# Kernel tuning notes

Measured on AMD Instinct MI355X. Metric: run time of the kernel, lower is better.

Reference implementation:

```python
import jax, jax.numpy as jnp
import numpy as np

BS, NQ, DIM, HEADS, POINTS, LEVELS = 2, 4096, 768, 6, 4, 1
HD = DIM // HEADS
H = W = 64
NV = H * W
EPS = 1e-6


def setup_inputs() -> dict:
    key = jax.random.key(0)
    ks = jax.random.split(key, 16)
    s = 0.02  # param init scale
    return {
        "query": jax.random.normal(ks[0], (BS, NQ, DIM), jnp.float32),
        "reference_points": jax.random.uniform(ks[1], (BS, NQ, LEVELS, 2), jnp.float32),
        "feat": jax.random.normal(ks[2], (BS, NV, DIM), jnp.float32),
        "spatial_shapes": np.array([[H, W]], dtype=np.int64),
        "level_start_index": np.array([0], dtype=np.int64),
        "ln_w": jnp.ones((DIM,), jnp.float32),
        "ln_b": jnp.zeros((DIM,), jnp.float32),
        "vp_w": jax.random.normal(ks[3], (DIM, DIM), jnp.float32) * s,
        "vp_b": jnp.zeros((DIM,), jnp.float32),
        "off_w": jax.random.normal(ks[4], (DIM, HEADS * LEVELS * POINTS * 2), jnp.float32) * s,
        "off_b": jax.random.normal(ks[5], (HEADS * LEVELS * POINTS * 2,), jnp.float32),
        "aw_w": jax.random.normal(ks[6], (DIM, HEADS * LEVELS * POINTS), jnp.float32) * s,
        "aw_b": jnp.zeros((HEADS * LEVELS * POINTS,), jnp.float32),
        "out_w": jax.random.normal(ks[7], (DIM, DIM), jnp.float32) * s,
        "out_b": jnp.zeros((DIM,), jnp.float32),
        "gamma": jax.random.normal(ks[8], (DIM,), jnp.float32) * 0.1,
    }


def _layernorm(x, w, b):
    mu = jnp.mean(x, axis=-1, keepdims=True)
    var = jnp.mean(jnp.square(x - mu), axis=-1, keepdims=True)
    return (x - mu) * jax.lax.rsqrt(var + EPS) * w + b


def _bilinear_sample(img, loc):
    # img: (bs, heads, H, W, hd); loc: (bs, nq, heads, points, 2) in [0,1]
    # matches torch.grid_sample(align_corners=False, padding_mode='zeros')
    bs, heads, h, w, hd = img.shape
    x = loc[..., 0] * w - 0.5
    y = loc[..., 1] * h - 0.5
    x0 = jnp.floor(x)
    y0 = jnp.floor(y)
    wx = x - x0
    wy = y - y0
    x0i = x0.astype(jnp.int32)
    y0i = y0.astype(jnp.int32)
    bi = jnp.arange(bs)[:, None, None, None]
    hi = jnp.arange(heads)[None, None, :, None]

    def gather(yi, xi):
        valid = (xi >= 0) & (xi < w) & (yi >= 0) & (yi < h)
        v = img[bi, hi, jnp.clip(yi, 0, h - 1), jnp.clip(xi, 0, w - 1)]
        return v * valid[..., None].astype(img.dtype)

    v00 = gather(y0i, x0i)
    v01 = gather(y0i, x0i + 1)
    v10 = gather(y0i + 1, x0i)
    v11 = gather(y0i + 1, x0i + 1)
    wx = wx[..., None]
    wy = wy[..., None]
    return (v00 * (1 - wy) * (1 - wx) + v01 * (1 - wy) * wx
            + v10 * wy * (1 - wx) + v11 * wy * wx)


def _msda(q, value, reference_points, spatial_shapes, off_w, off_b, aw_w, aw_b, out_w, out_b):
    bs, nq, _ = q.shape
    nv = value.shape[1]
    value = value.reshape(bs, nv, HEADS, HD)
    offsets = (q @ off_w + off_b).reshape(bs, nq, HEADS, LEVELS, POINTS, 2)
    aw = jax.nn.softmax(q @ aw_w + aw_b, axis=-1).reshape(bs, nq, HEADS, LEVELS, POINTS)
    # offset_normalizer = [W_l, H_l] per level
    norm = jnp.asarray(np.asarray(spatial_shapes)[:, ::-1], jnp.float32)  # (L, 2)
    loc = reference_points[:, :, None, :, None, :] + offsets / norm[None, None, None, :, None, :]
    # loc: (bs, nq, heads, levels, points, 2)
    out = jnp.zeros((bs, nq, HEADS, HD), jnp.float32)
    start = 0
    for l in range(LEVELS):
        h_l, w_l = int(spatial_shapes[l][0]), int(spatial_shapes[l][1])
        img = value[:, start:start + h_l * w_l].reshape(bs, h_l, w_l, HEADS, HD).transpose(0, 3, 1, 2, 4)
        sampled = _bilinear_sample(img, loc[:, :, :, l])  # (bs, nq, heads, points, hd)
        out = out + jnp.einsum('bnhpd,bnhp->bnhd', sampled, aw[:, :, :, l])
        start += h_l * w_l
    return out.reshape(bs, nq, DIM) @ out_w + out_b


def reference(query, reference_points, feat, spatial_shapes, level_start_index,
              ln_w, ln_b, vp_w, vp_b, off_w, off_b, aw_w, aw_b, out_w, out_b, gamma):
    q = _layernorm(query, ln_w, ln_b)
    value = feat @ vp_w + vp_b
    attn = _msda(q, value, reference_points, spatial_shapes,
                 off_w, off_b, aw_w, aw_b, out_w, out_b)
    # identity = zeros, dropout = 0 -> attn as-is; residual scale by gamma
    return query + gamma * attn
```

## Files before the change

### kernel.cpp

```cpp
#include <hip/hip_runtime.h>
#include <hip/hip_bf16.h>
#include <math.h>

#define BSZ 2
#define NQ 4096
#define DIM 768
#define HEADS 6
#define POINTS 4
#define HD 128
#define HW_DIM 64
#define NV (HW_DIM*HW_DIM)
#define M_TOTAL (BSZ*NQ)
#define KDIM 768
#define KSPLIT 2
#define KPART (KDIM/KSPLIT)

#define BM 64
#define BN 128
#define BKK 64
#define NBLK_M (M_TOTAL/BM)
#define NBLK_N (DIM/BN)
#define GEMM_GRID (NBLK_M*NBLK_N)
#define LN_BLOCKS (M_TOTAL/4)
#define TR_BLOCKS (576+576+72)

typedef __attribute__((ext_vector_type(8))) short bf16x8;
typedef __attribute__((ext_vector_type(4))) float f32x4;
typedef unsigned int u32;
typedef unsigned short u16;

__device__ inline u16 f2bf(float f) {
    union { float f; u32 u; } v; v.f = f;
    u32 r = v.u + 0x7fffu + ((v.u >> 16) & 1u);
    return (u16)(r >> 16);
}

#define GLD16(g, l) __builtin_amdgcn_global_load_lds( \
    (const __attribute__((address_space(1))) u32*)(g), \
    (__attribute__((address_space(3))) u32*)(l), 16, 0, 0)

__global__ __launch_bounds__(256) void prep_kernel(
        const float* __restrict__ x, const float* __restrict__ lnw,
        const float* __restrict__ lnb, u16* __restrict__ q,
        const float* __restrict__ feat, u16* __restrict__ feat_bf,
        const float* __restrict__ vp_w,  u16* __restrict__ vp_wt,
        const float* __restrict__ out_w, u16* __restrict__ out_wt,
        const float* __restrict__ off_w, const float* __restrict__ aw_w,
        u16* __restrict__ oaw_wt) {
    int b = blockIdx.x;
    if (b < LN_BLOCKS) {
        int wave = threadIdx.x >> 6, lane = threadIdx.x & 63;
        int row = b * 4 + wave;
        int c = lane * 4;
        const float* xr = x + (size_t)row * DIM;
        const float* fr = feat + (size_t)row * DIM;
        float4 v0 = *(const float4*)(xr + c);
        float4 v1 = *(const float4*)(xr + c + 256);
        float4 v2 = *(const float4*)(xr + c + 512);
        float4 f0 = *(const float4*)(fr + c);
        float4 f1 = *(const float4*)(fr + c + 256);
        float4 f2 = *(const float4*)(fr + c + 512);
        u16* fb = feat_bf + (size_t)row * DIM;
        ushort4 fo;
        fo.x = f2bf(f0.x); fo.y = f2bf(f0.y); fo.z = f2bf(f0.z); fo.w = f2bf(f0.w);
        *(ushort4*)(fb + c) = fo;
        fo.x = f2bf(f1.x); fo.y = f2bf(f1.y); fo.z = f2bf(f1.z); fo.w = f2bf(f1.w);
        *(ushort4*)(fb + c + 256) = fo;
        fo.x = f2bf(f2.x); fo.y = f2bf(f2.y); fo.z = f2bf(f2.z); fo.w = f2bf(f2.w);
        *(ushort4*)(fb + c + 512) = fo;

        float s  = v0.x+v0.y+v0.z+v0.w + v1.x+v1.y+v1.z+v1.w + v2.x+v2.y+v2.z+v2.w;
        float ss = v0.x*v0.x+v0.y*v0.y+v0.z*v0.z+v0.w*v0.w
                 + v1.x*v1.x+v1.y*v1.y+v1.z*v1.z+v1.w*v1.w
                 + v2.x*v2.x+v2.y*v2.y+v2.z*v2.z+v2.w*v2.w;
        #pragma unroll
        for (int st = 1; st < 64; st <<= 1) {
            s  += __shfl_xor(s,  st, 64);
            ss += __shfl_xor(ss, st, 64);
        }
        float mean = s * (1.0f / DIM);
        float var  = ss * (1.0f / DIM) - mean * mean;
        float rstd = rsqrtf(var + 1e-6f);
        u16* qr = q + (size_t)row * DIM;
        #pragma unroll
        for (int g = 0; g < 3; g++) {
            float4 v = (g == 0) ? v0 : (g == 1) ? v1 : v2;
            int cc = c + g * 256;
            const float4 ww = *(const float4*)(lnw + cc);
            const float4 bb = *(const float4*)(lnb + cc);
            ushort4 o;
            o.x = f2bf((v.x - mean) * rstd * ww.x + bb.x);
            o.y = f2bf((v.y - mean) * rstd * ww.y + bb.y);
            o.z = f2bf((v.z - mean) * rstd * ww.z + bb.z);
            o.w = f2bf((v.w - mean) * rstd * ww.w + bb.w);
            *(ushort4*)(qr + cc) = o;
        }
    } else {
        int t = b - LN_BLOCKS;
        int z, xk, yk;
        if (t < 576)      { z = 0; xk = t % 24; yk = t / 24; }
        else if (t < 1152){ z = 1; t -= 576; xk = t % 24; yk = t / 24; }
        else              { z = 2; t -= 1152; xk = t % 3; yk = t / 3; }
        __shared__ float tile[32][33];
        int n0 = xk * 32, k0 = yk * 32;
        int tx = threadIdx.x & 31, ty = threadIdx.x >> 5;
        const float* src = (z == 0) ? vp_w : (z == 1) ? out_w : nullptr;
        u16* dst = (z == 0) ? vp_wt : (z == 1) ? out_wt : oaw_wt;
        #pragma unroll
        for (int r = 0; r < 4; r++) {
            int k = k0 + ty + r * 8, n = n0 + tx;
            float v = 0.0f;
            if (z < 2) {
                v = src[(size_t)k * DIM + n];
            } else {
                if (n < 48) v = off_w[(size_t)k * 48 + n];
                else if (n < 72) v = aw_w[(size_t)k * 24 + (n - 48)];
            }
            tile[ty + r * 8][tx] = v;
        }
        __syncthreads();
        #pragma unroll
        for (int r = 0; r < 4; r++) {
            int nn = ty + r * 8, kk = tx;
            int drow = n0 + nn;
            if (z == 2 && drow >= 80) continue;
            dst[(size_t)drow * KDIM + k0 + kk] = f2bf(tile[kk][nn]);
        }
    }
}

__device__ __forceinline__ void gemm_big_body(int b,
        const u16* __restrict__ A, const u16* __restrict__ Bt,
        const float* __restrict__ bias, void* __restrict__ Cout,
        int storeBF16, const float* __restrict__ resid,
        const float* __restrict__ gamma) {
    __shared__ u16 As[BM * BKK];
    __shared__ u16 Bs[BN * BKK];
    int tid = threadIdx.x, w = tid >> 6, lane = tid & 63;
    int lm = lane & 15, quad = lane >> 4;
    int xcd = b & 7, idx = b >> 3;
    int mb = xcd * 16 + idx / NBLK_N;
    int nb = idx % NBLK_N;
    int m0 = mb * BM, n0 = nb * BN;
    int wr = w & 1, wc = w >> 1;

    int srow = lane >> 3;
    int scol = (lane & 7) ^ srow;
    const u16* Ab = A + (size_t)m0 * KDIM;
    const u16* Bb = Bt + (size_t)n0 * KDIM;

    f32x4 acc[2][4];
    #pragma unroll
    for (int i = 0; i < 2; i++)
        #pragma unroll
        for (int j = 0; j < 4; j++) acc[i][j] = (f32x4){0.f, 0.f, 0.f, 0.f};

    const u16* aaddr[2][2];
    const u16* baddr[4][2];
    #pragma unroll
    for (int i = 0; i < 2; i++) {
        int row = wr * 32 + i * 16 + lm;
        #pragma unroll
        for (int kk = 0; kk < 2; kk++)
            aaddr[i][kk] = &As[row * BKK + (((quad + 4 * kk) ^ (row & 7)) << 3)];
    }
    #pragma unroll
    for (int j = 0; j < 4; j++) {
        int row = wc * 64 + j * 16 + lm;
        #pragma unroll
        for (int kk = 0; kk < 2; kk++)
            baddr[j][kk] = &Bs[row * BKK + (((quad + 4 * kk) ^ (row & 7)) << 3)];
    }

    for (int k0 = 0; k0 < KDIM; k0 += BKK) {
        #pragma unroll
        for (int r = 0; r < 2; r++) {
            int row = r * 32 + w * 8 + srow;
            GLD16(Ab + (size_t)row * KDIM + k0 + scol * 8, &As[(r * 32 + w * 8) * BKK]);
        }
        #pragma unroll
        for (int r = 0; r < 4; r++) {
            int row = r * 32 + w * 8 + srow;
            GLD16(Bb + (size_t)row * KDIM + k0 + scol * 8, &Bs[(r * 32 + w * 8) * BKK]);
        }
        __syncthreads();
        #pragma unroll
        for (int kk = 0; kk < 2; kk++) {
            bf16x8 af[2], bf[4];
            #pragma unroll
            for (int i = 0; i < 2; i++) af[i] = *(const bf16x8*)aaddr[i][kk];
            #pragma unroll
            for (int j = 0; j < 4; j++) bf[j] = *(const bf16x8*)baddr[j][kk];
            #pragma unroll
            for (int i = 0; i < 2; i++)
                #pragma unroll
                for (int j = 0; j < 4; j++)
                    acc[i][j] = __builtin_amdgcn_mfma_f32_16x16x32_bf16(af[i], bf[j], acc[i][j], 0, 0, 0);
        }
        __syncthreads();
    }

    #pragma unroll
    for (int j = 0; j < 4; j++) {
        int col = n0 + wc * 64 + j * 16 + lm;
        float bb = bias[col];
        #pragma unroll
        for (int i = 0; i < 2; i++) {
            #pragma unroll
            for (int r = 0; r < 4; r++) {
                int row = m0 + wr * 32 + i * 16 + quad * 4 + r;
                size_t idxo = (size_t)row * DIM + col;
                float v = acc[i][j][r] + bb;
                if (storeBF16) {
                    ((u16*)Cout)[idxo] = f2bf(v);
                } else {
                    ((float*)Cout)[idxo] = resid[idxo] + gamma[col] * v;
                }
            }
        }
    }
}

__device__ __forceinline__ void gemm_small_body(int mblk, int part,
        const u16* __restrict__ A, const u16* __restrict__ Bt,
        const float* __restrict__ b0, const float* __restrict__ b1,
        float* __restrict__ C) {
    __shared__ u16 As2[64 * 32];
    __shared__ u16 Bs2[80 * 32];
    int tid = threadIdx.x, wave = tid >> 6, lane = tid & 63;
    int lm = lane & 15, quad = lane >> 4;
    int m0 = mblk * 64;
    int kbase = part * KPART;
    f32x4 acc[5];
    #pragma unroll
    for (int i = 0; i < 5; i++) acc[i] = (f32x4){0.f, 0.f, 0.f, 0.f};
    int lrow = lane >> 2, lcol = (lane & 3) * 8;

    for (int k0 = kbase; k0 < kbase + KPART; k0 += 32) {
        for (int c = wave; c < 9; c += 4) {
            if (c < 4) {
                GLD16(A + (size_t)(m0 + c * 16 + lrow) * KDIM + k0 + lcol, &As2[c * 16 * 32]);
            } else {
                GLD16(Bt + (size_t)((c - 4) * 16 + lrow) * KDIM + k0 + lcol, &Bs2[(c - 4) * 16 * 32]);
            }
        }
        __syncthreads();
        bf16x8 af = *(const bf16x8*)&As2[(wave * 16 + lm) * 32 + quad * 8];
        #pragma unroll
        for (int bn = 0; bn < 5; bn++) {
            bf16x8 bv = *(const bf16x8*)&Bs2[(bn * 16 + lm) * 32 + quad * 8];
            acc[bn] = __builtin_amdgcn_mfma_f32_16x16x32_bf16(af, bv, acc[bn], 0, 0, 0);
        }
        __syncthreads();
    }
    float* Cp = C + (size_t)part * M_TOTAL * 80;
    #pragma unroll
    for (int bn = 0; bn < 5; bn++) {
        int col = bn * 16 + lm;
        float bb = 0.0f;
        if (part == 0) bb = (col < 48) ? b0[col] : ((col < 72) ? b1[col - 48] : 0.0f);
        #pragma unroll
        for (int r = 0; r < 4; r++) {
            int row = m0 + wave * 16 + quad * 4 + r;
            Cp[(size_t)row * 80 + col] = acc[bn][r] + bb;
        }
    }
}

__global__ __launch_bounds__(256, 4) void gemms_kernel(
        const u16* __restrict__ feat_bf, const u16* __restrict__ vp_wt,
        const float* __restrict__ vp_b, u16* __restrict__ v_bf,
        const u16* __restrict__ q_bf, const u16* __restrict__ oaw_wt,
        const float* __restrict__ off_b, const float* __restrict__ aw_b,
        float* __restrict__ oa) {
    int b = blockIdx.x;
    if (b < GEMM_GRID) {
        gemm_big_body(b, feat_bf, vp_wt, vp_b, v_bf, 1, nullptr, nullptr);
    } else {
        int t = b - GEMM_GRID;
        gemm_small_body(t & 127, t >> 7, q_bf, oaw_wt, off_b, aw_b, oa);
    }
}

__global__ __launch_bounds__(256, 4) void outgemm_kernel(
        const u16* __restrict__ s_bf, const u16* __restrict__ out_wt,
        const float* __restrict__ out_b, float* __restrict__ out_f,
        const float* __restrict__ query, const float* __restrict__ gamma) {
    gemm_big_body(blockIdx.x, s_bf, out_wt, out_b, out_f, 0, query, gamma);
}

__global__ __launch_bounds__(192) void sample_kernel(
        const float* __restrict__ oa, const float* __restrict__ refp,
        const u16* __restrict__ v, u16* __restrict__ out) {
    int row = blockIdx.x;
    int b = row >> 12;
    int tid = threadIdx.x;
    __shared__ float s_w[4][24];
    __shared__ int   s_o[4][24];
    __shared__ float s_e[24];
    if (tid < 24) {
        int h = tid >> 2, p = tid & 3;
        float ox = 0.f, oy = 0.f, lg = 0.f;
        #pragma unroll
        for (int part = 0; part < KSPLIT; part++) {
            const float* pp = oa + (size_t)part * M_TOTAL * 80 + (size_t)row * 80;
            ox += pp[h * 8 + p * 2 + 0];
            oy += pp[h * 8 + p * 2 + 1];
            lg += pp[48 + tid];
        }
        float rx = refp[row * 2 + 0], ry = refp[row * 2 + 1];
        float x = (rx + ox * (1.0f / HW_DIM)) * HW_DIM - 0.5f;
        float y = (ry + oy * (1.0f / HW_DIM)) * HW_DIM - 0.5f;
        float fx = floorf(x), fy = floorf(y);
        int x0 = (int)fx, y0 = (int)fy;
        int x1 = x0 + 1, y1 = y0 + 1;
        float wx = x - fx, wy = y - fy;
        float vx0 = (x0 >= 0 && x0 < HW_DIM) ? 1.f : 0.f;
        float vx1 = (x1 >= 0 && x1 < HW_DIM) ? 1.f : 0.f;
        float vy0 = (y0 >= 0 && y0 < HW_DIM) ? 1.f : 0.f;
        float vy1 = (y1 >= 0 && y1 < HW_DIM) ? 1.f : 0.f;
        int xc0 = min(max(x0, 0), HW_DIM - 1), xc1 = min(max(x1, 0), HW_DIM - 1);
        int yc0 = min(max(y0, 0), HW_DIM - 1), yc1 = min(max(y1, 0), HW_DIM - 1);
        int base = b * NV * DIM;
        s_o[0][tid] = base + (yc0 * HW_DIM + xc0) * DIM;
        s_o[1][tid] = base + (yc0 * HW_DIM + xc1) * DIM;
        s_o[2][tid] = base + (yc1 * HW_DIM + xc0) * DIM;
        s_o[3][tid] = base + (yc1 * HW_DIM + xc1) * DIM;
        s_w[0][tid] = (1.f - wy) * (1.f - wx) * vy0 * vx0;
        s_w[1][tid] = (1.f - wy) * wx * vy0 * vx1;
        s_w[2][tid] = wy * (1.f - wx) * vy1 * vx0;
        s_w[3][tid] = wy * wx * vy1 * vx1;
        s_e[tid] = lg;
        float m = s_e[0];
        #pragma unroll
        for (int i = 1; i < 24; i++) m = fmaxf(m, s_e[i]);
        s_e[tid] = expf(lg - m);
    }
    __syncthreads();
    float ssum = 0.0f;
    #pragma unroll
    for (int i = 0; i < 24; i++) ssum += s_e[i];
    float inv = 1.0f / ssum;

    int h = tid >> 5;
    int d4 = (tid & 31) * 4;
    const u16* vb = v + h * HD + d4;
    float a0 = 0.f, a1 = 0.f, a2 = 0.f, a3 = 0.f;
    #pragma unroll
    for (int p = 0; p < 4; p++) {
        int idx = h * 4 + p;
        float aw = s_e[idx] * inv;
        #pragma unroll
        for (int c = 0; c < 4; c++) {
            uint2 u = *(const uint2*)(vb + s_o[c][idx]);
            float w = aw * s_w[c][idx];
            a0 += w * __uint_as_float(u.x << 16);
            a1 += w * __uint_as_float(u.x & 0xffff0000u);
            a2 += w * __uint_as_float(u.y << 16);
            a3 += w * __uint_as_float(u.y & 0xffff0000u);
        }
    }
    uint2 pack;
    pack.x = (u32)f2bf(a0) | ((u32)f2bf(a1) << 16);
    pack.y = (u32)f2bf(a2) | ((u32)f2bf(a3) << 16);
    *(uint2*)&out[(size_t)row * DIM + h * HD + d4] = pack;
}

extern "C" void kernel_launch(void* const* d_in, const int* in_sizes, int n_in,
                              void* d_out, int out_size, void* d_ws, size_t ws_size,
                              hipStream_t stream) {
    const float* query = (const float*)d_in[0];
    const float* refp  = (const float*)d_in[1];
    const float* feat  = (const float*)d_in[2];
    const float* ln_w  = (const float*)d_in[5];
    const float* ln_b  = (const float*)d_in[6];
    const float* vp_w  = (const float*)d_in[7];
    const float* vp_b  = (const float*)d_in[8];
    const float* off_w = (const float*)d_in[9];
    const float* off_b = (const float*)d_in[10];
    const float* aw_w  = (const float*)d_in[11];
    const float* aw_b  = (const float*)d_in[12];
    const float* out_w = (const float*)d_in[13];
    const float* out_b = (const float*)d_in[14];
    const float* gamma = (const float*)d_in[15];

    const size_t MD = (size_t)M_TOTAL * DIM;
    char* ws = (char*)d_ws;
    u16* q_bf    = (u16*)ws;                 ws += MD * 2;
    u16* feat_bf = (u16*)ws;                 ws += MD * 2;
    u16* v_bf    = (u16*)ws;                 ws += MD * 2;
    u16* s_bf    = (u16*)ws;                 ws += MD * 2;
    u16* vp_wt   = (u16*)ws;                 ws += (size_t)DIM * DIM * 2;
    u16* out_wt  = (u16*)ws;                 ws += (size_t)DIM * DIM * 2;
    u16* oaw_wt  = (u16*)ws;                 ws += (size_t)80 * KDIM * 2;
    float* oa    = (float*)ws;               ws += (size_t)KSPLIT * M_TOTAL * 80 * 4;
    float* out_f = (float*)d_out;

    prep_kernel<<<LN_BLOCKS + TR_BLOCKS, 256, 0, stream>>>(
        query, ln_w, ln_b, q_bf, feat, feat_bf,
        vp_w, vp_wt, out_w, out_wt, off_w, aw_w, oaw_wt);
    gemms_kernel<<<GEMM_GRID + 128 * KSPLIT, 256, 0, stream>>>(
        feat_bf, vp_wt, vp_b, v_bf, q_bf, oaw_wt, off_b, aw_b, oa);
    sample_kernel<<<M_TOTAL, 192, 0, stream>>>(oa, refp, v_bf, s_bf);
    outgemm_kernel<<<GEMM_GRID, 256, 0, stream>>>(s_bf, out_wt, out_b, out_f, query, gamma);
}
```

Before: 177.4 us.

## Restructure bilinear sampling into per-head multi-query blocks with shuffle softmax

The sampling kernel now assigns each block 16 queries for a single batch, head and half of the head's channels, instead of one block per query covering all heads. Each 16-lane group computes the 24-way softmax with warp shuffles instead of a shared-memory serial loop, and folds the attention weight into the bilinear weights. The aim is to cut per-block setup overhead and serial softmax work, and to improve occupancy with larger blocks. In exchange, each block redundantly recomputes the softmax for all heads, and gathers become narrower per query.

```diff
diff --git a/kernel.cpp b/kernel.cpp
--- a/kernel.cpp
+++ b/kernel.cpp
@@ -289,25 +289,45 @@
     gemm_big_body(blockIdx.x, s_bf, out_wt, out_b, out_f, 0, query, gamma);
 }
 
-__global__ __launch_bounds__(192) void sample_kernel(
+#define SMP_QPB 16
+#define SMP_COMBOS 24
+#define SMP_BLOCKS (SMP_COMBOS * (NQ / SMP_QPB))
+
+__global__ __launch_bounds__(256) void sample_kernel(
         const float* __restrict__ oa, const float* __restrict__ refp,
         const u16* __restrict__ v, u16* __restrict__ out) {
-    int row = blockIdx.x;
-    int b = row >> 12;
-    int tid = threadIdx.x;
-    __shared__ float s_w[4][24];
-    __shared__ int   s_o[4][24];
-    __shared__ float s_e[24];
-    if (tid < 24) {
-        int h = tid >> 2, p = tid & 3;
-        float ox = 0.f, oy = 0.f, lg = 0.f;
-        #pragma unroll
-        for (int part = 0; part < KSPLIT; part++) {
-            const float* pp = oa + (size_t)part * M_TOTAL * 80 + (size_t)row * 80;
-            ox += pp[h * 8 + p * 2 + 0];
-            oy += pp[h * 8 + p * 2 + 1];
-            lg += pp[48 + tid];
-        }
+    int combo = blockIdx.x % SMP_COMBOS;
+    int qblk  = blockIdx.x / SMP_COMBOS;
+    int head  = combo % 6;
+    int rest  = combo / 6;
+    int batch = rest >> 1;
+    int half  = rest & 1;
+    int tid  = threadIdx.x;
+    int q    = tid >> 4;
+    int lane = tid & 15;
+    int row  = batch * NQ + qblk * SMP_QPB + q;
+
+    __shared__ float s_w[SMP_QPB][4][4];
+    __shared__ int   s_o[SMP_QPB][4][4];
+
+    const float* p0 = oa + (size_t)row * 80;
+    const float* p1 = p0 + (size_t)M_TOTAL * 80;
+    float la = p0[48 + lane] + p1[48 + lane];
+    float lb = (lane < 8) ? (p0[64 + lane] + p1[64 + lane]) : -1e30f;
+    float m = fmaxf(la, lb);
+    #pragma unroll
+    for (int st = 1; st < 16; st <<= 1) m = fmaxf(m, __shfl_xor(m, st, 64));
+    float s = expf(la - m) + ((lane < 8) ? expf(lb - m) : 0.f);
+    #pragma unroll
+    for (int st = 1; st < 16; st <<= 1) s += __shfl_xor(s, st, 64);
+    float inv = 1.0f / s;
+
+    if (lane < 4) {
+        int p = lane;
+        float ox = p0[head * 8 + p * 2 + 0] + p1[head * 8 + p * 2 + 0];
+        float oy = p0[head * 8 + p * 2 + 1] + p1[head * 8 + p * 2 + 1];
+        float lg = p0[48 + head * 4 + p]    + p1[48 + head * 4 + p];
+        float aw = expf(lg - m) * inv;
         float rx = refp[row * 2 + 0], ry = refp[row * 2 + 1];
         float x = (rx + ox * (1.0f / HW_DIM)) * HW_DIM - 0.5f;
         float y = (ry + oy * (1.0f / HW_DIM)) * HW_DIM - 0.5f;
@@ -321,39 +341,27 @@
         float vy1 = (y1 >= 0 && y1 < HW_DIM) ? 1.f : 0.f;
         int xc0 = min(max(x0, 0), HW_DIM - 1), xc1 = min(max(x1, 0), HW_DIM - 1);
         int yc0 = min(max(y0, 0), HW_DIM - 1), yc1 = min(max(y1, 0), HW_DIM - 1);
-        int base = b * NV * DIM;
-        s_o[0][tid] = base + (yc0 * HW_DIM + xc0) * DIM;
-        s_o[1][tid] = base + (yc0 * HW_DIM + xc1) * DIM;
-        s_o[2][tid] = base + (yc1 * HW_DIM + xc0) * DIM;
-        s_o[3][tid] = base + (yc1 * HW_DIM + xc1) * DIM;
-        s_w[0][tid] = (1.f - wy) * (1.f - wx) * vy0 * vx0;
-        s_w[1][tid] = (1.f - wy) * wx * vy0 * vx1;
-        s_w[2][tid] = wy * (1.f - wx) * vy1 * vx0;
-        s_w[3][tid] = wy * wx * vy1 * vx1;
-        s_e[tid] = lg;
-        float m = s_e[0];
-        #pragma unroll
-        for (int i = 1; i < 24; i++) m = fmaxf(m, s_e[i]);
-        s_e[tid] = expf(lg - m);
+        int base = batch * NV * DIM;
+        s_o[q][p][0] = base + (yc0 * HW_DIM + xc0) * DIM;
+        s_o[q][p][1] = base + (yc0 * HW_DIM + xc1) * DIM;
+        s_o[q][p][2] = base + (yc1 * HW_DIM + xc0) * DIM;
+        s_o[q][p][3] = base + (yc1 * HW_DIM + xc1) * DIM;
+        s_w[q][p][0] = aw * (1.f - wy) * (1.f - wx) * vy0 * vx0;
+        s_w[q][p][1] = aw * (1.f - wy) * wx * vy0 * vx1;
+        s_w[q][p][2] = aw * wy * (1.f - wx) * vy1 * vx0;
+        s_w[q][p][3] = aw * wy * wx * vy1 * vx1;
     }
     __syncthreads();
-    float ssum = 0.0f;
-    #pragma unroll
-    for (int i = 0; i < 24; i++) ssum += s_e[i];
-    float inv = 1.0f / ssum;
-
-    int h = tid >> 5;
-    int d4 = (tid & 31) * 4;
-    const u16* vb = v + h * HD + d4;
+
+    int dbase = head * HD + half * 64 + lane * 4;
+    const u16* vb = v + dbase;
     float a0 = 0.f, a1 = 0.f, a2 = 0.f, a3 = 0.f;
     #pragma unroll
     for (int p = 0; p < 4; p++) {
-        int idx = h * 4 + p;
-        float aw = s_e[idx] * inv;
         #pragma unroll
         for (int c = 0; c < 4; c++) {
-            uint2 u = *(const uint2*)(vb + s_o[c][idx]);
-            float w = aw * s_w[c][idx];
+            float w = s_w[q][p][c];
+            uint2 u = *(const uint2*)(vb + s_o[q][p][c]);
             a0 += w * __uint_as_float(u.x << 16);
             a1 += w * __uint_as_float(u.x & 0xffff0000u);
             a2 += w * __uint_as_float(u.y << 16);
@@ -363,7 +371,7 @@
     uint2 pack;
     pack.x = (u32)f2bf(a0) | ((u32)f2bf(a1) << 16);
     pack.y = (u32)f2bf(a2) | ((u32)f2bf(a3) << 16);
-    *(uint2*)&out[(size_t)row * DIM + h * HD + d4] = pack;
+    *(uint2*)&out[(size_t)row * DIM + dbase] = pack;
 }
 
 extern "C" void kernel_launch(void* const* d_in, const int* in_sizes, int n_in,
@@ -401,6 +409,6 @@
         vp_w, vp_wt, out_w, out_wt, off_w, aw_w, oaw_wt);
     gemms_kernel<<<GEMM_GRID + 128 * KSPLIT, 256, 0, stream>>>(
         feat_bf, vp_wt, vp_b, v_bf, q_bf, oaw_wt, off_b, aw_b, oa);
-    sample_kernel<<<M_TOTAL, 192, 0, stream>>>(oa, refp, v_bf, s_bf);
+    sample_kernel<<<SMP_BLOCKS, 256, 0, stream>>>(oa, refp, v_bf, s_bf);
     outgemm_kernel<<<GEMM_GRID, 256, 0, stream>>>(s_bf, out_wt, out_b, out_f, query, gamma);
 }
```

After: 180.8 us. Within noise of the previous version (+2.0%).

## Fuse LayerNorm into the offset/attention-weight GEMM and drop its K-split

Applied to the files above, without the earlier changes.

LayerNorm on the query moves out of the prep kernel and into the small offset/attention-weight GEMM. Each block now computes per-row mean and rstd, then normalises and converts fp32 query tiles to bf16 directly into LDS, so the bf16 q buffer is never written or read back. The K-split of 2 is removed, so each block covers the full K=768 and the sample kernel no longer sums two partial outputs. In exchange, the small GEMM runs half as many blocks, each with twice the K-loop, and reads the query in fp32 twice (once for the statistics, once for the tiles). It also no longer uses async global-to-LDS loads for A.

```diff
diff --git a/kernel.cpp b/kernel.cpp
--- a/kernel.cpp
+++ b/kernel.cpp
@@ -12,8 +12,6 @@
 #define NV (HW_DIM*HW_DIM)
 #define M_TOTAL (BSZ*NQ)
 #define KDIM 768
-#define KSPLIT 2
-#define KPART (KDIM/KSPLIT)
 
 #define BM 64
 #define BN 128
@@ -21,8 +19,9 @@
 #define NBLK_M (M_TOTAL/BM)
 #define NBLK_N (DIM/BN)
 #define GEMM_GRID (NBLK_M*NBLK_N)
-#define LN_BLOCKS (M_TOTAL/4)
+#define CVT_BLOCKS (M_TOTAL/4)
 #define TR_BLOCKS (576+576+72)
+#define SMALL_BLOCKS (M_TOTAL/64)
 
 typedef __attribute__((ext_vector_type(8))) short bf16x8;
 typedef __attribute__((ext_vector_type(4))) float f32x4;
@@ -40,23 +39,17 @@
     (__attribute__((address_space(3))) u32*)(l), 16, 0, 0)
 
 __global__ __launch_bounds__(256) void prep_kernel(
-        const float* __restrict__ x, const float* __restrict__ lnw,
-        const float* __restrict__ lnb, u16* __restrict__ q,
         const float* __restrict__ feat, u16* __restrict__ feat_bf,
         const float* __restrict__ vp_w,  u16* __restrict__ vp_wt,
         const float* __restrict__ out_w, u16* __restrict__ out_wt,
         const float* __restrict__ off_w, const float* __restrict__ aw_w,
         u16* __restrict__ oaw_wt) {
     int b = blockIdx.x;
-    if (b < LN_BLOCKS) {
+    if (b < CVT_BLOCKS) {
         int wave = threadIdx.x >> 6, lane = threadIdx.x & 63;
         int row = b * 4 + wave;
         int c = lane * 4;
-        const float* xr = x + (size_t)row * DIM;
         const float* fr = feat + (size_t)row * DIM;
-        float4 v0 = *(const float4*)(xr + c);
-        float4 v1 = *(const float4*)(xr + c + 256);
-        float4 v2 = *(const float4*)(xr + c + 512);
         float4 f0 = *(const float4*)(fr + c);
         float4 f1 = *(const float4*)(fr + c + 256);
         float4 f2 = *(const float4*)(fr + c + 512);
@@ -68,35 +61,8 @@
         *(ushort4*)(fb + c + 256) = fo;
         fo.x = f2bf(f2.x); fo.y = f2bf(f2.y); fo.z = f2bf(f2.z); fo.w = f2bf(f2.w);
         *(ushort4*)(fb + c + 512) = fo;
-
-        float s  = v0.x+v0.y+v0.z+v0.w + v1.x+v1.y+v1.z+v1.w + v2.x+v2.y+v2.z+v2.w;
-        float ss = v0.x*v0.x+v0.y*v0.y+v0.z*v0.z+v0.w*v0.w
-                 + v1.x*v1.x+v1.y*v1.y+v1.z*v1.z+v1.w*v1.w
-                 + v2.x*v2.x+v2.y*v2.y+v2.z*v2.z+v2.w*v2.w;
-        #pragma unroll
-        for (int st = 1; st < 64; st <<= 1) {
-            s  += __shfl_xor(s,  st, 64);
-            ss += __shfl_xor(ss, st, 64);
-        }
-        float mean = s * (1.0f / DIM);
-        float var  = ss * (1.0f / DIM) - mean * mean;
-        float rstd = rsqrtf(var + 1e-6f);
-        u16* qr = q + (size_t)row * DIM;
-        #pragma unroll
-        for (int g = 0; g < 3; g++) {
-            float4 v = (g == 0) ? v0 : (g == 1) ? v1 : v2;
-            int cc = c + g * 256;
-            const float4 ww = *(const float4*)(lnw + cc);
-            const float4 bb = *(const float4*)(lnb + cc);
-            ushort4 o;
-            o.x = f2bf((v.x - mean) * rstd * ww.x + bb.x);
-            o.y = f2bf((v.y - mean) * rstd * ww.y + bb.y);
-            o.z = f2bf((v.z - mean) * rstd * ww.z + bb.z);
-            o.w = f2bf((v.w - mean) * rstd * ww.w + bb.w);
-            *(ushort4*)(qr + cc) = o;
-        }
     } else {
-        int t = b - LN_BLOCKS;
+        int t = b - CVT_BLOCKS;
         int z, xk, yk;
         if (t < 576)      { z = 0; xk = t % 24; yk = t / 24; }
         else if (t < 1152){ z = 1; t -= 576; xk = t % 24; yk = t / 24; }
@@ -221,28 +187,74 @@
     }
 }
 
-__device__ __forceinline__ void gemm_small_body(int mblk, int part,
-        const u16* __restrict__ A, const u16* __restrict__ Bt,
+__device__ __forceinline__ void gemm_small_body(int mblk,
+        const float* __restrict__ query, const float* __restrict__ lnw,
+        const float* __restrict__ lnb, const u16* __restrict__ Bt,
         const float* __restrict__ b0, const float* __restrict__ b1,
         float* __restrict__ C) {
     __shared__ u16 As2[64 * 32];
     __shared__ u16 Bs2[80 * 32];
+    __shared__ float s_mu[64], s_rs[64];
     int tid = threadIdx.x, wave = tid >> 6, lane = tid & 63;
     int lm = lane & 15, quad = lane >> 4;
     int m0 = mblk * 64;
-    int kbase = part * KPART;
+
+    #pragma unroll 4
+    for (int it = 0; it < 16; it++) {
+        int row = it * 4 + wave;
+        const float* xr = query + (size_t)(m0 + row) * DIM + lane * 4;
+        float4 v0 = *(const float4*)(xr);
+        float4 v1 = *(const float4*)(xr + 256);
+        float4 v2 = *(const float4*)(xr + 512);
+        float s  = v0.x+v0.y+v0.z+v0.w + v1.x+v1.y+v1.z+v1.w + v2.x+v2.y+v2.z+v2.w;
+        float ss = v0.x*v0.x+v0.y*v0.y+v0.z*v0.z+v0.w*v0.w
+                 + v1.x*v1.x+v1.y*v1.y+v1.z*v1.z+v1.w*v1.w
+                 + v2.x*v2.x+v2.y*v2.y+v2.z*v2.z+v2.w*v2.w;
+        #pragma unroll
+        for (int st = 1; st < 64; st <<= 1) {
+            s  += __shfl_xor(s,  st, 64);
+            ss += __shfl_xor(ss, st, 64);
+        }
+        if (lane == 0) {
+            float mean = s * (1.0f / DIM);
+            float var  = ss * (1.0f / DIM) - mean * mean;
+            s_mu[row] = mean;
+            s_rs[row] = rsqrtf(var + 1e-6f);
+        }
+    }
+    __syncthreads();
+
     f32x4 acc[5];
     #pragma unroll
     for (int i = 0; i < 5; i++) acc[i] = (f32x4){0.f, 0.f, 0.f, 0.f};
+    int arow = tid >> 2;
+    int acol = (tid & 3) * 8;
     int lrow = lane >> 2, lcol = (lane & 3) * 8;
 
-    for (int k0 = kbase; k0 < kbase + KPART; k0 += 32) {
-        for (int c = wave; c < 9; c += 4) {
-            if (c < 4) {
-                GLD16(A + (size_t)(m0 + c * 16 + lrow) * KDIM + k0 + lcol, &As2[c * 16 * 32]);
-            } else {
-                GLD16(Bt + (size_t)((c - 4) * 16 + lrow) * KDIM + k0 + lcol, &Bs2[(c - 4) * 16 * 32]);
-            }
+    for (int k0 = 0; k0 < KDIM; k0 += 32) {
+        {
+            const float* xr = query + (size_t)(m0 + arow) * DIM + k0 + acol;
+            float4 a = *(const float4*)xr;
+            float4 b = *(const float4*)(xr + 4);
+            float4 w0 = *(const float4*)(lnw + k0 + acol);
+            float4 w1 = *(const float4*)(lnw + k0 + acol + 4);
+            float4 c0 = *(const float4*)(lnb + k0 + acol);
+            float4 c1 = *(const float4*)(lnb + k0 + acol + 4);
+            float mu = s_mu[arow], rs = s_rs[arow];
+            ushort4 o0, o1;
+            o0.x = f2bf((a.x - mu) * rs * w0.x + c0.x);
+            o0.y = f2bf((a.y - mu) * rs * w0.y + c0.y);
+            o0.z = f2bf((a.z - mu) * rs * w0.z + c0.z);
+            o0.w = f2bf((a.w - mu) * rs * w0.w + c0.w);
+            o1.x = f2bf((b.x - mu) * rs * w1.x + c1.x);
+            o1.y = f2bf((b.y - mu) * rs * w1.y + c1.y);
+            o1.z = f2bf((b.z - mu) * rs * w1.z + c1.z);
+            o1.w = f2bf((b.w - mu) * rs * w1.w + c1.w);
+            *(ushort4*)&As2[arow * 32 + acol]     = o0;
+            *(ushort4*)&As2[arow * 32 + acol + 4] = o1;
+        }
+        for (int c = wave; c < 5; c += 4) {
+            GLD16(Bt + (size_t)(c * 16 + lrow) * KDIM + k0 + lcol, &Bs2[c * 16 * 32]);
         }
         __syncthreads();
         bf16x8 af = *(const bf16x8*)&As2[(wave * 16 + lm) * 32 + quad * 8];
@@ -253,16 +265,14 @@
         }
         __syncthreads();
     }
-    float* Cp = C + (size_t)part * M_TOTAL * 80;
     #pragma unroll
     for (int bn = 0; bn < 5; bn++) {
         int col = bn * 16 + lm;
-        float bb = 0.0f;
-        if (part == 0) bb = (col < 48) ? b0[col] : ((col < 72) ? b1[col - 48] : 0.0f);
+        float bb = (col < 48) ? b0[col] : ((col < 72) ? b1[col - 48] : 0.0f);
         #pragma unroll
         for (int r = 0; r < 4; r++) {
             int row = m0 + wave * 16 + quad * 4 + r;
-            Cp[(size_t)row * 80 + col] = acc[bn][r] + bb;
+            C[(size_t)row * 80 + col] = acc[bn][r] + bb;
         }
     }
 }
@@ -270,15 +280,15 @@
 __global__ __launch_bounds__(256, 4) void gemms_kernel(
         const u16* __restrict__ feat_bf, const u16* __restrict__ vp_wt,
         const float* __restrict__ vp_b, u16* __restrict__ v_bf,
-        const u16* __restrict__ q_bf, const u16* __restrict__ oaw_wt,
+        const float* __restrict__ query, const float* __restrict__ lnw,
+        const float* __restrict__ lnb, const u16* __restrict__ oaw_wt,
         const float* __restrict__ off_b, const float* __restrict__ aw_b,
         float* __restrict__ oa) {
     int b = blockIdx.x;
     if (b < GEMM_GRID) {
         gemm_big_body(b, feat_bf, vp_wt, vp_b, v_bf, 1, nullptr, nullptr);
     } else {
-        int t = b - GEMM_GRID;
-        gemm_small_body(t & 127, t >> 7, q_bf, oaw_wt, off_b, aw_b, oa);
+        gemm_small_body(b - GEMM_GRID, query, lnw, lnb, oaw_wt, off_b, aw_b, oa);
     }
 }
 
@@ -300,14 +310,10 @@
     __shared__ float s_e[24];
     if (tid < 24) {
         int h = tid >> 2, p = tid & 3;
-        float ox = 0.f, oy = 0.f, lg = 0.f;
-        #pragma unroll
-        for (int part = 0; part < KSPLIT; part++) {
-            const float* pp = oa + (size_t)part * M_TOTAL * 80 + (size_t)row * 80;
-            ox += pp[h * 8 + p * 2 + 0];
-            oy += pp[h * 8 + p * 2 + 1];
-            lg += pp[48 + tid];
-        }
+        const float* pp = oa + (size_t)row * 80;
+        float ox = pp[h * 8 + p * 2 + 0];
+        float oy = pp[h * 8 + p * 2 + 1];
+        float lg = pp[48 + tid];
         float rx = refp[row * 2 + 0], ry = refp[row * 2 + 1];
         float x = (rx + ox * (1.0f / HW_DIM)) * HW_DIM - 0.5f;
         float y = (ry + oy * (1.0f / HW_DIM)) * HW_DIM - 0.5f;
@@ -386,21 +392,19 @@
 
     const size_t MD = (size_t)M_TOTAL * DIM;
     char* ws = (char*)d_ws;
-    u16* q_bf    = (u16*)ws;                 ws += MD * 2;
     u16* feat_bf = (u16*)ws;                 ws += MD * 2;
     u16* v_bf    = (u16*)ws;                 ws += MD * 2;
     u16* s_bf    = (u16*)ws;                 ws += MD * 2;
     u16* vp_wt   = (u16*)ws;                 ws += (size_t)DIM * DIM * 2;
     u16* out_wt  = (u16*)ws;                 ws += (size_t)DIM * DIM * 2;
     u16* oaw_wt  = (u16*)ws;                 ws += (size_t)80 * KDIM * 2;
-    float* oa    = (float*)ws;               ws += (size_t)KSPLIT * M_TOTAL * 80 * 4;
+    float* oa    = (float*)ws;               ws += (size_t)M_TOTAL * 80 * 4;
     float* out_f = (float*)d_out;
 
-    prep_kernel<<<LN_BLOCKS + TR_BLOCKS, 256, 0, stream>>>(
-        query, ln_w, ln_b, q_bf, feat, feat_bf,
-        vp_w, vp_wt, out_w, out_wt, off_w, aw_w, oaw_wt);
-    gemms_kernel<<<GEMM_GRID + 128 * KSPLIT, 256, 0, stream>>>(
-        feat_bf, vp_wt, vp_b, v_bf, q_bf, oaw_wt, off_b, aw_b, oa);
+    prep_kernel<<<CVT_BLOCKS + TR_BLOCKS, 256, 0, stream>>>(
+        feat, feat_bf, vp_w, vp_wt, out_w, out_wt, off_w, aw_w, oaw_wt);
+    gemms_kernel<<<GEMM_GRID + SMALL_BLOCKS, 256, 0, stream>>>(
+        feat_bf, vp_wt, vp_b, v_bf, query, ln_w, ln_b, oaw_wt, off_b, aw_b, oa);
     sample_kernel<<<M_TOTAL, 192, 0, stream>>>(oa, refp, v_bf, s_bf);
     outgemm_kernel<<<GEMM_GRID, 256, 0, stream>>>(s_bf, out_wt, out_b, out_f, query, gamma);
 }
```

Result: slower. 196.8 us (+11.0%).

## Double-buffer LDS tiles in the GEMM kernels to overlap loads with MFMA

Applied to the files above, without the earlier changes.

Both the large and small bf16 GEMM bodies now use two LDS buffers for each operand. The next K-tile is issued via global_load_lds while MFMAs run on the current one, replacing the load-sync-compute-sync sequence. The goal is to hide global-to-LDS latency behind compute. In exchange, shared memory per block roughly doubles, to a single dynamic-sized array shared across branches, and launch bounds drop from 4 to 3 blocks per CU, which lowers occupancy.

```diff
diff --git a/kernel.cpp b/kernel.cpp
--- a/kernel.cpp
+++ b/kernel.cpp
@@ -23,6 +23,10 @@
 #define GEMM_GRID (NBLK_M*NBLK_N)
 #define LN_BLOCKS (M_TOTAL/4)
 #define TR_BLOCKS (576+576+72)
+
+#define A_TILE (BM*BKK)
+#define B_TILE (BN*BKK)
+#define SMEM_U16 (2*(A_TILE+B_TILE))
 
 typedef __attribute__((ext_vector_type(8))) short bf16x8;
 typedef __attribute__((ext_vector_type(4))) float f32x4;
@@ -129,13 +133,13 @@
     }
 }
 
-__device__ __forceinline__ void gemm_big_body(int b,
+__device__ __forceinline__ void gemm_big_body(int b, u16* __restrict__ smem,
         const u16* __restrict__ A, const u16* __restrict__ Bt,
         const float* __restrict__ bias, void* __restrict__ Cout,
         int storeBF16, const float* __restrict__ resid,
         const float* __restrict__ gamma) {
-    __shared__ u16 As[BM * BKK];
-    __shared__ u16 Bs[BN * BKK];
+    u16* As = smem;
+    u16* Bs = smem + 2 * A_TILE;
     int tid = threadIdx.x, w = tid >> 6, lane = tid & 63;
     int lm = lane & 15, quad = lane >> 4;
     int xcd = b & 7, idx = b >> 3;
@@ -155,42 +159,51 @@
         #pragma unroll
         for (int j = 0; j < 4; j++) acc[i][j] = (f32x4){0.f, 0.f, 0.f, 0.f};
 
-    const u16* aaddr[2][2];
-    const u16* baddr[4][2];
+    int aoff[2][2], boff[4][2];
     #pragma unroll
     for (int i = 0; i < 2; i++) {
         int row = wr * 32 + i * 16 + lm;
         #pragma unroll
         for (int kk = 0; kk < 2; kk++)
-            aaddr[i][kk] = &As[row * BKK + (((quad + 4 * kk) ^ (row & 7)) << 3)];
+            aoff[i][kk] = row * BKK + (((quad + 4 * kk) ^ (row & 7)) << 3);
     }
     #pragma unroll
     for (int j = 0; j < 4; j++) {
         int row = wc * 64 + j * 16 + lm;
         #pragma unroll
         for (int kk = 0; kk < 2; kk++)
-            baddr[j][kk] = &Bs[row * BKK + (((quad + 4 * kk) ^ (row & 7)) << 3)];
-    }
-
-    for (int k0 = 0; k0 < KDIM; k0 += BKK) {
+            boff[j][kk] = row * BKK + (((quad + 4 * kk) ^ (row & 7)) << 3);
+    }
+
+    auto stage = [&](int buf, int k0) {
         #pragma unroll
         for (int r = 0; r < 2; r++) {
             int row = r * 32 + w * 8 + srow;
-            GLD16(Ab + (size_t)row * KDIM + k0 + scol * 8, &As[(r * 32 + w * 8) * BKK]);
+            GLD16(Ab + (size_t)row * KDIM + k0 + scol * 8,
+                  As + buf * A_TILE + (r * 32 + w * 8) * BKK);
         }
         #pragma unroll
         for (int r = 0; r < 4; r++) {
             int row = r * 32 + w * 8 + srow;
-            GLD16(Bb + (size_t)row * KDIM + k0 + scol * 8, &Bs[(r * 32 + w * 8) * BKK]);
-        }
-        __syncthreads();
+            GLD16(Bb + (size_t)row * KDIM + k0 + scol * 8,
+                  Bs + buf * B_TILE + (r * 32 + w * 8) * BKK);
+        }
+    };
+
+    stage(0, 0);
+    __syncthreads();
+    const int NT = KDIM / BKK;
+    for (int t = 0; t < NT; t++) {
+        if (t + 1 < NT) stage((t + 1) & 1, (t + 1) * BKK);
+        const u16* Ap = As + (t & 1) * A_TILE;
+        const u16* Bp = Bs + (t & 1) * B_TILE;
         #pragma unroll
         for (int kk = 0; kk < 2; kk++) {
             bf16x8 af[2], bf[4];
             #pragma unroll
-            for (int i = 0; i < 2; i++) af[i] = *(const bf16x8*)aaddr[i][kk];
+            for (int i = 0; i < 2; i++) af[i] = *(const bf16x8*)(Ap + aoff[i][kk]);
             #pragma unroll
-            for (int j = 0; j < 4; j++) bf[j] = *(const bf16x8*)baddr[j][kk];
+            for (int j = 0; j < 4; j++) bf[j] = *(const bf16x8*)(Bp + boff[j][kk]);
             #pragma unroll
             for (int i = 0; i < 2; i++)
                 #pragma unroll
@@ -221,12 +234,15 @@
     }
 }
 
+#define SA_TILE (64*32)
+#define SB_TILE (80*32)
 __device__ __forceinline__ void gemm_small_body(int mblk, int part,
+        u16* __restrict__ smem,
         const u16* __restrict__ A, const u16* __restrict__ Bt,
         const float* __restrict__ b0, const float* __restrict__ b1,
         float* __restrict__ C) {
-    __shared__ u16 As2[64 * 32];
-    __shared__ u16 Bs2[80 * 32];
+    u16* As2 = smem;
+    u16* Bs2 = smem + 2 * SA_TILE;
     int tid = threadIdx.x, wave = tid >> 6, lane = tid & 63;
     int lm = lane & 15, quad = lane >> 4;
     int m0 = mblk * 64;
@@ -236,19 +252,29 @@
     for (int i = 0; i < 5; i++) acc[i] = (f32x4){0.f, 0.f, 0.f, 0.f};
     int lrow = lane >> 2, lcol = (lane & 3) * 8;
 
-    for (int k0 = kbase; k0 < kbase + KPART; k0 += 32) {
+    auto stage = [&](int buf, int k0) {
         for (int c = wave; c < 9; c += 4) {
             if (c < 4) {
-                GLD16(A + (size_t)(m0 + c * 16 + lrow) * KDIM + k0 + lcol, &As2[c * 16 * 32]);
+                GLD16(A + (size_t)(m0 + c * 16 + lrow) * KDIM + k0 + lcol,
+                      As2 + buf * SA_TILE + c * 16 * 32);
             } else {
-                GLD16(Bt + (size_t)((c - 4) * 16 + lrow) * KDIM + k0 + lcol, &Bs2[(c - 4) * 16 * 32]);
+                GLD16(Bt + (size_t)((c - 4) * 16 + lrow) * KDIM + k0 + lcol,
+                      Bs2 + buf * SB_TILE + (c - 4) * 16 * 32);
             }
         }
-        __syncthreads();
-        bf16x8 af = *(const bf16x8*)&As2[(wave * 16 + lm) * 32 + quad * 8];
+    };
+
+    stage(0, kbase);
+    __syncthreads();
+    const int NT = KPART / 32;
+    for (int t = 0; t < NT; t++) {
+        if (t + 1 < NT) stage((t + 1) & 1, kbase + (t + 1) * 32);
+        const u16* Ap = As2 + (t & 1) * SA_TILE;
+        const u16* Bp = Bs2 + (t & 1) * SB_TILE;
+        bf16x8 af = *(const bf16x8*)(Ap + (wave * 16 + lm) * 32 + quad * 8);
         #pragma unroll
         for (int bn = 0; bn < 5; bn++) {
-            bf16x8 bv = *(const bf16x8*)&Bs2[(bn * 16 + lm) * 32 + quad * 8];
+            bf16x8 bv = *(const bf16x8*)(Bp + (bn * 16 + lm) * 32 + quad * 8);
             acc[bn] = __builtin_amdgcn_mfma_f32_16x16x32_bf16(af, bv, acc[bn], 0, 0, 0);
         }
         __syncthreads();
@@ -267,26 +293,28 @@
     }
 }
 
-__global__ __launch_bounds__(256, 4) void gemms_kernel(
+__global__ __launch_bounds__(256, 3) void gemms_kernel(
         const u16* __restrict__ feat_bf, const u16* __restrict__ vp_wt,
         const float* __restrict__ vp_b, u16* __restrict__ v_bf,
         const u16* __restrict__ q_bf, const u16* __restrict__ oaw_wt,
         const float* __restrict__ off_b, const float* __restrict__ aw_b,
         float* __restrict__ oa) {
+    __shared__ u16 smem[SMEM_U16];
     int b = blockIdx.x;
     if (b < GEMM_GRID) {
-        gemm_big_body(b, feat_bf, vp_wt, vp_b, v_bf, 1, nullptr, nullptr);
+        gemm_big_body(b, smem, feat_bf, vp_wt, vp_b, v_bf, 1, nullptr, nullptr);
     } else {
         int t = b - GEMM_GRID;
-        gemm_small_body(t & 127, t >> 7, q_bf, oaw_wt, off_b, aw_b, oa);
-    }
-}
-
-__global__ __launch_bounds__(256, 4) void outgemm_kernel(
+        gemm_small_body(t & 127, t >> 7, smem, q_bf, oaw_wt, off_b, aw_b, oa);
+    }
+}
+
+__global__ __launch_bounds__(256, 3) void outgemm_kernel(
         const u16* __restrict__ s_bf, const u16* __restrict__ out_wt,
         const float* __restrict__ out_b, float* __restrict__ out_f,
         const float* __restrict__ query, const float* __restrict__ gamma) {
-    gemm_big_body(blockIdx.x, s_bf, out_wt, out_b, out_f, 0, query, gamma);
+    __shared__ u16 smem[SMEM_U16];
+    gemm_big_body(blockIdx.x, smem, s_bf, out_wt, out_b, out_f, 0, query, gamma);
 }
 
 __global__ __launch_bounds__(192) void sample_kernel(
```

Result: no change. 176.9 us (-0.3%).
